# Kernel tuning notes

Hardware: AMD Instinct MI355X
Metric: run time of the kernel (lower is better)

## Reference

```python
import jax, jax.numpy as jnp
import numpy as np

B, L, F = 8, 4096, 64  # batch, max_len, feat_dim (in_features == out_features)


def setup_inputs() -> dict:
    key = jax.random.key(0)
    k1, k2, k3, k4 = jax.random.split(key, 4)
    text = jax.random.normal(k1, (B, L, F), dtype=jnp.float32)
    adj = jax.random.uniform(k2, (B, L, L), dtype=jnp.float32)
    weight = jax.random.normal(k3, (F, F), dtype=jnp.float32) * (1.0 / np.sqrt(F))
    bias = jax.random.normal(k4, (F,), dtype=jnp.float32) * 0.01
    return {"text": text, "adj": adj, "weight": weight, "bias": bias}


def reference(text, adj, weight, bias):
    # Original: out[b,i,:] = sum_j adj[b,i,j] * (text[b,j,:] @ W) + bias
    # i.e. adj @ (text @ W) + bias, without the wasteful [B,L,L,F] intermediate.
    hidden = jnp.einsum('blf,fo->blo', text, weight)      # [B,L,F]
    out = jnp.einsum('bij,bjo->bio', adj, hidden)          # [B,L,F]
    return out + bias
```

## Files before the change

### kernel.cpp

```cpp
#include <hip/hip_runtime.h>
#include <hip/hip_bf16.h>

#define LDIM 4096
#define FDIM 64
#define BM 64
#define BK 64
#define NIT (LDIM / BK)

typedef __attribute__((ext_vector_type(8))) __bf16 bf16x8;
typedef __attribute__((ext_vector_type(4))) float f32x4;

__device__ __forceinline__ unsigned short f2bf(float f) {
    unsigned int u = __float_as_uint(f);
    u += 0x7fffu + ((u >> 16) & 1u);
    return (unsigned short)(u >> 16);
}

__global__ __launch_bounds__(256) void hidden_kernel(
    const float* __restrict__ text, const float* __restrict__ weight,
    unsigned short* __restrict__ hT)
{
    const int b  = blockIdx.x & 7;
    const int lc = blockIdx.x >> 3;
    const int l0 = lc * 64;
    __shared__ float sw[64 * 64];
    __shared__ float st[64 * 65];
    const int t = threadIdx.x;
    #pragma unroll
    for (int i = 0; i < 16; ++i) sw[t + i * 256] = weight[t + i * 256];
    const float* tp = text + ((size_t)b * LDIM + l0) * FDIM;
    #pragma unroll
    for (int i = 0; i < 16; ++i) {
        int idx = t + i * 256;
        st[(idx >> 6) * 65 + (idx & 63)] = tp[idx];
    }
    __syncthreads();
    const int l  = t & 63;
    const int o0 = (t >> 6) * 16;
    float acc[16];
    #pragma unroll
    for (int i = 0; i < 16; ++i) acc[i] = 0.f;
    for (int f = 0; f < 64; ++f) {
        float tv = st[l * 65 + f];
        #pragma unroll
        for (int i = 0; i < 16; ++i) acc[i] += tv * sw[f * 64 + o0 + i];
    }
    unsigned short* hp = hT + ((size_t)b * FDIM + o0) * LDIM + l0 + l;
    #pragma unroll
    for (int i = 0; i < 16; ++i) hp[(size_t)i * LDIM] = f2bf(acc[i]);
}

__global__ __launch_bounds__(256, 2) void gemm_kernel(
    const float* __restrict__ adj, const unsigned short* __restrict__ hT,
    const float* __restrict__ bias, float* __restrict__ out)
{
    const int b  = blockIdx.x & 7;
    const int mb = blockIdx.x >> 3;
    const int m0 = mb * BM;
    const int tid  = threadIdx.x;
    const int w    = tid >> 6;
    const int lane = tid & 63;

    __shared__ __align__(16) unsigned short sA[BM * 72];
    __shared__ __align__(16) unsigned short sB[64 * 72];

    const float*          abase = adj + ((size_t)b * LDIM + m0) * LDIM;
    const unsigned short* hbase = hT + (size_t)b * FDIM * LDIM;

    const int am = tid >> 4;
    const int ac = tid & 15;
    const int bn = tid >> 3;
    const int bg = tid & 7;

    float4 aCur[4]; uint4 bCur[2];
    #pragma unroll
    for (int i = 0; i < 4; ++i)
        aCur[i] = *(const float4*)(abase + (size_t)(am + 16 * i) * LDIM + ac * 4);
    #pragma unroll
    for (int i = 0; i < 2; ++i)
        bCur[i] = *(const uint4*)(hbase + (size_t)(bn + 32 * i) * LDIM + bg * 8);

    f32x4 acc[4];
    #pragma unroll
    for (int nf = 0; nf < 4; ++nf) acc[nf] = (f32x4){0.f, 0.f, 0.f, 0.f};

    const int fm = lane & 15;
    const int fq = lane >> 4;

    for (int it = 0; it < NIT; ++it) {
        __syncthreads();
        #pragma unroll
        for (int i = 0; i < 4; ++i) {
            union { unsigned short us[4]; uint2 v; } pk;
            pk.us[0] = f2bf(aCur[i].x); pk.us[1] = f2bf(aCur[i].y);
            pk.us[2] = f2bf(aCur[i].z); pk.us[3] = f2bf(aCur[i].w);
            *(uint2*)&sA[(am + 16 * i) * 72 + ac * 4] = pk.v;
        }
        #pragma unroll
        for (int i = 0; i < 2; ++i)
            *(uint4*)&sB[(bn + 32 * i) * 72 + bg * 8] = bCur[i];
        __syncthreads();

        float4 aNxt[4]; uint4 bNxt[2];
        const int nk = (it + 1) * BK;
        const bool more = (it + 1 < NIT);
        if (more) {
            #pragma unroll
            for (int i = 0; i < 4; ++i)
                aNxt[i] = *(const float4*)(abase + (size_t)(am + 16 * i) * LDIM + nk + ac * 4);
            #pragma unroll
            for (int i = 0; i < 2; ++i)
                bNxt[i] = *(const uint4*)(hbase + (size_t)(bn + 32 * i) * LDIM + nk + bg * 8);
        }

        #pragma unroll
        for (int kf = 0; kf < 2; ++kf) {
            bf16x8 af = *(const bf16x8*)&sA[(w * 16 + fm) * 72 + kf * 32 + fq * 8];
            #pragma unroll
            for (int nf = 0; nf < 4; ++nf) {
                bf16x8 bfr = *(const bf16x8*)&sB[(nf * 16 + fm) * 72 + kf * 32 + fq * 8];
                acc[nf] = __builtin_amdgcn_mfma_f32_16x16x32_bf16(af, bfr, acc[nf], 0, 0, 0);
            }
        }

        if (more) {
            #pragma unroll
            for (int i = 0; i < 4; ++i) aCur[i] = aNxt[i];
            #pragma unroll
            for (int i = 0; i < 2; ++i) bCur[i] = bNxt[i];
        }
    }

    float* obase = out + ((size_t)b * LDIM + m0 + w * 16 + fq * 4) * FDIM + fm;
    #pragma unroll
    for (int nf = 0; nf < 4; ++nf) {
        float bv = bias[nf * 16 + fm];
        #pragma unroll
        for (int r = 0; r < 4; ++r)
            obase[(size_t)r * FDIM + nf * 16] = acc[nf][r] + bv;
    }
}

extern "C" void kernel_launch(void* const* d_in, const int* in_sizes, int n_in,
                              void* d_out, int out_size, void* d_ws, size_t ws_size,
                              hipStream_t stream) {
    const float* text   = (const float*)d_in[0];
    const float* adj    = (const float*)d_in[1];
    const float* weight = (const float*)d_in[2];
    const float* bias   = (const float*)d_in[3];
    float* out = (float*)d_out;
    unsigned short* hT = (unsigned short*)d_ws;

    hidden_kernel<<<512, 256, 0, stream>>>(text, weight, hT);
    gemm_kernel<<<512, 256, 0, stream>>>(adj, hT, bias, out);
}
```

Measured before the change: 741.5 us.

## Load MFMA fragments directly from global memory, drop shared-memory staging

After: 773.6 us. 1.04x slower.

```diff
diff --git a/kernel.cpp b/kernel.cpp
--- a/kernel.cpp
+++ b/kernel.cpp
@@ -3,9 +3,7 @@
 
 #define LDIM 4096
 #define FDIM 64
-#define BM 64
-#define BK 64
-#define NIT (LDIM / BK)
+#define NIT 64
 
 typedef __attribute__((ext_vector_type(8))) __bf16 bf16x8;
 typedef __attribute__((ext_vector_type(4))) float f32x4;
@@ -14,6 +12,14 @@
     unsigned int u = __float_as_uint(f);
     u += 0x7fffu + ((u >> 16) & 1u);
     return (unsigned short)(u >> 16);
+}
+
+__device__ __forceinline__ unsigned int pk2bf(float lo, float hi) {
+    unsigned int ul = __float_as_uint(lo);
+    ul += 0x7fffu + ((ul >> 16) & 1u);
+    unsigned int uh = __float_as_uint(hi);
+    uh += 0x7fffu + ((uh >> 16) & 1u);
+    return (ul >> 16) | (uh & 0xffff0000u);
 }
 
 __global__ __launch_bounds__(256) void hidden_kernel(
@@ -56,85 +62,64 @@
 {
     const int b  = blockIdx.x & 7;
     const int mb = blockIdx.x >> 3;
-    const int m0 = mb * BM;
-    const int tid  = threadIdx.x;
-    const int w    = tid >> 6;
-    const int lane = tid & 63;
+    const int w    = threadIdx.x >> 6;
+    const int lane = threadIdx.x & 63;
+    const int m16  = lane & 15;
+    const int q    = lane >> 4;
 
-    __shared__ __align__(16) unsigned short sA[BM * 72];
-    __shared__ __align__(16) unsigned short sB[64 * 72];
+    const int m0 = mb * 64 + w * 16;
+    const float* arow = adj + ((size_t)b * LDIM + m0 + m16) * LDIM + q * 8;
+    const unsigned short* hrow = hT + ((size_t)b * FDIM + m16) * LDIM + q * 8;
 
-    const float*          abase = adj + ((size_t)b * LDIM + m0) * LDIM;
-    const unsigned short* hbase = hT + (size_t)b * FDIM * LDIM;
+    float4 aL[2][2], aH[2][2];
+    uint4  bf_[2][8];
 
-    const int am = tid >> 4;
-    const int ac = tid & 15;
-    const int bn = tid >> 3;
-    const int bg = tid & 7;
-
-    float4 aCur[4]; uint4 bCur[2];
-    #pragma unroll
-    for (int i = 0; i < 4; ++i)
-        aCur[i] = *(const float4*)(abase + (size_t)(am + 16 * i) * LDIM + ac * 4);
-    #pragma unroll
-    for (int i = 0; i < 2; ++i)
-        bCur[i] = *(const uint4*)(hbase + (size_t)(bn + 32 * i) * LDIM + bg * 8);
+    auto loadT = [&](int buf, int kk) {
+        #pragma unroll
+        for (int ks = 0; ks < 2; ++ks) {
+            aL[buf][ks] = *(const float4*)(arow + kk + ks * 32);
+            aH[buf][ks] = *(const float4*)(arow + kk + ks * 32 + 4);
+        }
+        #pragma unroll
+        for (int nf = 0; nf < 4; ++nf)
+            #pragma unroll
+            for (int ks = 0; ks < 2; ++ks)
+                bf_[buf][nf * 2 + ks] =
+                    *(const uint4*)(hrow + (size_t)nf * 16 * LDIM + kk + ks * 32);
+    };
 
     f32x4 acc[4];
     #pragma unroll
     for (int nf = 0; nf < 4; ++nf) acc[nf] = (f32x4){0.f, 0.f, 0.f, 0.f};
 
-    const int fm = lane & 15;
-    const int fq = lane >> 4;
+    loadT(0, 0);
 
+    #pragma unroll 2
     for (int it = 0; it < NIT; ++it) {
-        __syncthreads();
-        #pragma unroll
-        for (int i = 0; i < 4; ++i) {
-            union { unsigned short us[4]; uint2 v; } pk;
-            pk.us[0] = f2bf(aCur[i].x); pk.us[1] = f2bf(aCur[i].y);
-            pk.us[2] = f2bf(aCur[i].z); pk.us[3] = f2bf(aCur[i].w);
-            *(uint2*)&sA[(am + 16 * i) * 72 + ac * 4] = pk.v;
-        }
-        #pragma unroll
-        for (int i = 0; i < 2; ++i)
-            *(uint4*)&sB[(bn + 32 * i) * 72 + bg * 8] = bCur[i];
-        __syncthreads();
-
-        float4 aNxt[4]; uint4 bNxt[2];
-        const int nk = (it + 1) * BK;
-        const bool more = (it + 1 < NIT);
-        if (more) {
-            #pragma unroll
-            for (int i = 0; i < 4; ++i)
-                aNxt[i] = *(const float4*)(abase + (size_t)(am + 16 * i) * LDIM + nk + ac * 4);
-            #pragma unroll
-            for (int i = 0; i < 2; ++i)
-                bNxt[i] = *(const uint4*)(hbase + (size_t)(bn + 32 * i) * LDIM + nk + bg * 8);
-        }
+        const int cur = it & 1, nxt = cur ^ 1;
+        const int nk = (it + 1 < NIT) ? (it + 1) * 64 : 0;
+        loadT(nxt, nk);
 
         #pragma unroll
-        for (int kf = 0; kf < 2; ++kf) {
-            bf16x8 af = *(const bf16x8*)&sA[(w * 16 + fm) * 72 + kf * 32 + fq * 8];
+        for (int ks = 0; ks < 2; ++ks) {
+            union { unsigned int u[4]; bf16x8 v; } af;
+            af.u[0] = pk2bf(aL[cur][ks].x, aL[cur][ks].y);
+            af.u[1] = pk2bf(aL[cur][ks].z, aL[cur][ks].w);
+            af.u[2] = pk2bf(aH[cur][ks].x, aH[cur][ks].y);
+            af.u[3] = pk2bf(aH[cur][ks].z, aH[cur][ks].w);
             #pragma unroll
             for (int nf = 0; nf < 4; ++nf) {
-                bf16x8 bfr = *(const bf16x8*)&sB[(nf * 16 + fm) * 72 + kf * 32 + fq * 8];
-                acc[nf] = __builtin_amdgcn_mfma_f32_16x16x32_bf16(af, bfr, acc[nf], 0, 0, 0);
+                union { uint4 u; bf16x8 v; } bv;
+                bv.u = bf_[cur][nf * 2 + ks];
+                acc[nf] = __builtin_amdgcn_mfma_f32_16x16x32_bf16(af.v, bv.v, acc[nf], 0, 0, 0);
             }
-        }
-
-        if (more) {
-            #pragma unroll
-            for (int i = 0; i < 4; ++i) aCur[i] = aNxt[i];
-            #pragma unroll
-            for (int i = 0; i < 2; ++i) bCur[i] = bNxt[i];
         }
     }
 
-    float* obase = out + ((size_t)b * LDIM + m0 + w * 16 + fq * 4) * FDIM + fm;
+    float* obase = out + ((size_t)b * LDIM + m0 + q * 4) * FDIM + m16;
     #pragma unroll
     for (int nf = 0; nf < 4; ++nf) {
-        float bv = bias[nf * 16 + fm];
+        float bv = bias[nf * 16 + m16];
         #pragma unroll
         for (int r = 0; r < 4; ++r)
             obase[(size_t)r * FDIM + nf * 16] = acc[nf][r] + bv;
```
